# Kernel optimization log

Hardware: AMD Instinct MI355X
Metric: run time of the kernel (lower is better)

## Reference

```python
import jax, jax.numpy as jnp
import numpy as np

B, S, T, D = 4, 512, 512, 256


def setup_inputs() -> dict:
    key = jax.random.key(0)
    ks = jax.random.split(key, 10)
    scale = 1.0 / np.sqrt(D)
    return {
        "source": jax.random.normal(ks[0], (B, S, D), jnp.float32),
        "target": jax.random.normal(ks[1], (B, T, D), jnp.float32),
        "W_src": jax.random.uniform(ks[2], (D, D), jnp.float32, -scale, scale),
        "b_src": jax.random.uniform(ks[3], (D,), jnp.float32, -scale, scale),
        "W_tgt": jax.random.uniform(ks[4], (D, D), jnp.float32, -scale, scale),
        "b_tgt": jax.random.uniform(ks[5], (D,), jnp.float32, -scale, scale),
        "W_res": jax.random.uniform(ks[6], (D, 1), jnp.float32, -scale, scale),
        "b_res": jax.random.uniform(ks[7], (1,), jnp.float32, -scale, scale),
        "W_prob": jax.random.uniform(ks[8], (D, 2), jnp.float32, -scale, scale),
        "b_prob": jax.random.uniform(ks[9], (2,), jnp.float32, -scale, scale),
    }


def reference(source, target, W_src, b_src, W_tgt, b_tgt, W_res, b_res, W_prob, b_prob):
    # source: (B,S,D), target: (B,T,D)
    src_lin = jnp.einsum("bsd,de->bse", source, W_src) + b_src  # (B,S,D)
    tgt_lin = jnp.einsum("btd,de->bte", target, W_tgt) + b_tgt  # (B,T,D)
    # Bahdanau-style additive attention: (B,T,S,D) broadcast, tanh, D->1
    h = jnp.tanh(src_lin[:, None, :, :] + tgt_lin[:, :, None, :])  # (B,T,S,D)
    genP = jnp.einsum("btsd,d->bts", h, W_res[:, 0]) + b_res[0]     # (B,T,S)
    prob = jax.nn.softmax(jnp.einsum("btd,de->bte", target, W_prob) + b_prob, axis=-1)  # (B,T,2)
    return genP, prob
```

## Files before the change

### kernel.cpp

```cpp
#include <hip/hip_runtime.h>

#define B_ 4
#define S_ 512
#define T_ 512
#define D_ 256
#define NSRC (B_ * S_)
#define K2F 2.8853900817779268f

typedef __attribute__((ext_vector_type(8))) short short8;
typedef __attribute__((ext_vector_type(4))) float f32x4;
typedef __attribute__((ext_vector_type(2))) float f32x2;

__device__ __forceinline__ unsigned short f2bf(float f) {
    union { float f; unsigned u; } v; v.f = f;
    unsigned r = v.u + 0x7FFF + ((v.u >> 16) & 1);
    return (unsigned short)(r >> 16);
}

__global__ __launch_bounds__(256) void prep_kernel(
    const float* __restrict__ tgt,
    const float* __restrict__ Wsrc, const float* __restrict__ Wtgt,
    const float* __restrict__ Wp, const float* __restrict__ bp,
    unsigned short* __restrict__ wtb, float* __restrict__ out)
{
    __shared__ float tl[64 * 65];
    const int blk = blockIdx.x, tid = threadIdx.x;

    if (blk < 32) {
        int wb = blk;
        int e = wb >> 4, ti = wb & 15, tr = ti >> 2, tc = ti & 3;
        int r0 = tr * 64, c0 = tc * 64;
        const float* W = e ? Wtgt : Wsrc;
        #pragma unroll
        for (int it = 0; it < 4; it++) {
            int rr = (tid >> 4) + it * 16;
            int cc = (tid & 15) * 4;
            float4 v = *(const float4*)&W[(r0 + rr) * D_ + c0 + cc];
            tl[(cc + 0) * 65 + rr] = v.x;
            tl[(cc + 1) * 65 + rr] = v.y;
            tl[(cc + 2) * 65 + rr] = v.z;
            tl[(cc + 3) * 65 + rr] = v.w;
        }
        __syncthreads();
        #pragma unroll
        for (int it = 0; it < 2; it++) {
            int jj = (tid >> 3) + it * 32;
            int kk = (tid & 7) * 8;
            ushort4 lo, hi;
            lo.x = f2bf(tl[jj * 65 + kk + 0]); lo.y = f2bf(tl[jj * 65 + kk + 1]);
            lo.z = f2bf(tl[jj * 65 + kk + 2]); lo.w = f2bf(tl[jj * 65 + kk + 3]);
            hi.x = f2bf(tl[jj * 65 + kk + 4]); hi.y = f2bf(tl[jj * 65 + kk + 5]);
            hi.z = f2bf(tl[jj * 65 + kk + 6]); hi.w = f2bf(tl[jj * 65 + kk + 7]);
            int idx = (e * 256 + c0 + jj) * D_ + r0 + kk;
            *(ushort4*)&wtb[idx] = lo;
            *(ushort4*)&wtb[idx + 4] = hi;
        }
    } else {
        int row  = (blk - 32) * 4 + (tid >> 6);
        int lane = tid & 63;
        float p0 = 0.f, p1 = 0.f;
        #pragma unroll
        for (int i = 0; i < 4; i++) {
            int d = lane + i * 64;
            float v = tgt[row * D_ + d];
            float2 w = *(const float2*)&Wp[d * 2];
            p0 = fmaf(v, w.x, p0);
            p1 = fmaf(v, w.y, p1);
        }
        #pragma unroll
        for (int off = 32; off > 0; off >>= 1) {
            p0 += __shfl_down(p0, off, 64);
            p1 += __shfl_down(p1, off, 64);
        }
        if (lane == 0) {
            const float L2E = 1.4426950408889634f;
            float l0 = p0 + bp[0], l1 = p1 + bp[1];
            float e10 = __builtin_amdgcn_exp2f((l1 - l0) * L2E);
            float e01 = __builtin_amdgcn_exp2f((l0 - l1) * L2E);
            out[B_ * T_ * S_ + row * 2 + 0] = __builtin_amdgcn_rcpf(1.f + e10);
            out[B_ * T_ * S_ + row * 2 + 1] = __builtin_amdgcn_rcpf(1.f + e01);
        }
    }
}

#define LSTR 68
__global__ __launch_bounds__(768, 1) void mega_kernel(
    const float* __restrict__ src, const float* __restrict__ tgt,
    const unsigned short* __restrict__ wtb,
    const float* __restrict__ bsrc, const float* __restrict__ btgt,
    const float* __restrict__ Wres, const float* __restrict__ bres,
    float* __restrict__ out)
{
    __shared__ float ls[2][64 * LSTR];
    __shared__ float lt[2][64 * LSTR];
    __shared__ float c0s;

    const int tid = threadIdx.x;
    const int lane = tid & 63, w = tid >> 6;
    const int s0 = blockIdx.x * 64;
    const int t0 = blockIdx.y * 64;
    const int b  = blockIdx.z;

    if (w == 0) {
        float s = Wres[lane] + Wres[lane + 64] + Wres[lane + 128] + Wres[lane + 192];
        #pragma unroll
        for (int off = 32; off > 0; off >>= 1) s += __shfl_xor(s, off, 64);
        if (lane == 0) c0s = s + bres[0];
    }

    const bool producer = (w < 4);

    const int pw  = w & 3;
    const int mat = pw >> 1;
    const int rb  = 2 * (pw & 1);
    const int n = lane & 15, quad = lane >> 4;
    const float* bias = mat ? btgt : bsrc;
    const unsigned short* wtbase = wtb + mat * 256 * D_;

    short8 af[2][8];
    if (producer) {
        const float* xb = mat ? &tgt[(b * T_ + t0) * D_] : &src[(b * S_ + s0) * D_];
        #pragma unroll
        for (int rg = 0; rg < 2; rg++)
            #pragma unroll
            for (int ks = 0; ks < 8; ks++) {
                const float* p = &xb[((rb + rg) * 16 + n) * D_ + ks * 32 + quad * 8];
                float4 u0 = *(const float4*)p;
                float4 u1 = *(const float4*)(p + 4);
                short8 v;
                v[0] = (short)f2bf(u0.x); v[1] = (short)f2bf(u0.y);
                v[2] = (short)f2bf(u0.z); v[3] = (short)f2bf(u0.w);
                v[4] = (short)f2bf(u1.x); v[5] = (short)f2bf(u1.y);
                v[6] = (short)f2bf(u1.z); v[7] = (short)f2bf(u1.w);
                af[rg][ks] = v;
            }
    }

    auto phaseA = [&](int c, int bi) {
        float* lx = (mat ? lt[bi] : ls[bi]);
        #pragma unroll
        for (int cg = 0; cg < 4; cg++) {
            const int gcol = c * 4 + cg;
            const unsigned short* bptr = &wtbase[(gcol * 16 + n) * D_ + quad * 8];
            short8 bf[8];
            #pragma unroll
            for (int ks = 0; ks < 8; ks++) bf[ks] = *(const short8*)&bptr[ks * 32];
            const int dloc = cg * 16 + n;
            const float bv = bias[gcol * 16 + n];
            #pragma unroll
            for (int rg = 0; rg < 2; rg++) {
                f32x4 a4 = {0.f, 0.f, 0.f, 0.f};
                #pragma unroll
                for (int ks = 0; ks < 8; ks++)
                    a4 = __builtin_amdgcn_mfma_f32_16x16x32_bf16(af[rg][ks], bf[ks], a4, 0, 0, 0);
                float4 o;
                o.x = __builtin_amdgcn_exp2f((a4[0] + bv) * K2F);
                o.y = __builtin_amdgcn_exp2f((a4[1] + bv) * K2F);
                o.z = __builtin_amdgcn_exp2f((a4[2] + bv) * K2F);
                o.w = __builtin_amdgcn_exp2f((a4[3] + bv) * K2F);
                *(float4*)&lx[dloc * LSTR + (rb + rg) * 16 + quad * 4] = o;
            }
        }
    };

    const int cl = tid - 256;
    const int m = cl & 15;
    const int g = cl >> 4;
    f32x2 acc[2][2];
    #pragma unroll
    for (int i = 0; i < 2; i++) {
        acc[i][0] = (f32x2){0.f, 0.f};
        acc[i][1] = (f32x2){0.f, 0.f};
    }

    if (producer) phaseA(0, 0);
    __syncthreads();

    for (int c = 0; c < 4; c++) {
        const int bi = c & 1;
        if (producer) {
            if (c < 3) phaseA(c + 1, bi ^ 1);
        } else {
            const float* lsb = ls[bi];
            const float* ltb = lt[bi];
            const float* wp = &Wres[c * 64];
            const f32x2 one2 = {1.f, 1.f};
            #pragma unroll 2
            for (int kq = 0; kq < 8; kq++) {
                const int d0 = 8 * kq;
                f32x2 ap[8][2];
                float cc[8][2];
                f32x2 wv[8];
                #pragma unroll
                for (int k = 0; k < 8; k++) {
                    float4 a4 = *(const float4*)&lsb[(d0 + k) * LSTR + 4 * m];
                    float2 c2 = *(const float2*)&ltb[(d0 + k) * LSTR + 2 * g];
                    ap[k][0] = (f32x2){a4.x, a4.y};
                    ap[k][1] = (f32x2){a4.z, a4.w};
                    cc[k][0] = c2.x; cc[k][1] = c2.y;
                    const float wk = wp[d0 + k];
                    wv[k] = (f32x2){wk, wk};
                }
                #pragma unroll
                for (int i = 0; i < 2; i++) {
                    #pragma unroll
                    for (int jp = 0; jp < 2; jp++) {
                        f32x2 dd[8];
                        #pragma unroll
                        for (int k = 0; k < 8; k++) {
                            const f32x2 cs = {cc[k][i], cc[k][i]};
                            dd[k] = ap[k][jp] * cs + one2;
                        }
                        f32x2 p01 = dd[0] * dd[1];
                        f32x2 p23 = dd[2] * dd[3];
                        f32x2 p45 = dd[4] * dd[5];
                        f32x2 p67 = dd[6] * dd[7];
                        f32x2 q03 = p01 * p23;
                        f32x2 q47 = p45 * p67;
                        f32x2 den = q03 * q47;
                        f32x2 u01 = dd[1] * wv[0]; u01 = dd[0] * wv[1] + u01;
                        f32x2 u23 = dd[3] * wv[2]; u23 = dd[2] * wv[3] + u23;
                        f32x2 u45 = dd[5] * wv[4]; u45 = dd[4] * wv[5] + u45;
                        f32x2 u67 = dd[7] * wv[6]; u67 = dd[6] * wv[7] + u67;
                        f32x2 n03 = u01 * p23; n03 = u23 * p01 + n03;
                        f32x2 n47 = u45 * p67; n47 = u67 * p45 + n47;
                        f32x2 num = n03 * q47; num = n47 * q03 + num;
                        f32x2 r;
                        r.x = __builtin_amdgcn_rcpf(den.x);
                        r.y = __builtin_amdgcn_rcpf(den.y);
                        acc[i][jp] = num * r + acc[i][jp];
                    }
                }
            }
        }
        __syncthreads();
    }

    if (!producer) {
        const float C0 = c0s;
        #pragma unroll
        for (int i = 0; i < 2; i++) {
            float4 o;
            o.x = C0 - 2.f * acc[i][0].x;
            o.y = C0 - 2.f * acc[i][0].y;
            o.z = C0 - 2.f * acc[i][1].x;
            o.w = C0 - 2.f * acc[i][1].y;
            *(float4*)&out[(b * T_ + t0 + 2 * g + i) * S_ + s0 + 4 * m] = o;
        }
    }
}

extern "C" void kernel_launch(void* const* d_in, const int* in_sizes, int n_in,
                              void* d_out, int out_size, void* d_ws, size_t ws_size,
                              hipStream_t stream) {
    const float* source = (const float*)d_in[0];
    const float* target = (const float*)d_in[1];
    const float* W_src  = (const float*)d_in[2];
    const float* b_src  = (const float*)d_in[3];
    const float* W_tgt  = (const float*)d_in[4];
    const float* b_tgt  = (const float*)d_in[5];
    const float* W_res  = (const float*)d_in[6];
    const float* b_res  = (const float*)d_in[7];
    const float* W_prob = (const float*)d_in[8];
    const float* b_prob = (const float*)d_in[9];
    float* out = (float*)d_out;

    unsigned short* wtb = (unsigned short*)d_ws;

    prep_kernel<<<544, 256, 0, stream>>>(target, W_src, W_tgt,
                                         W_prob, b_prob, wtb, out);
    mega_kernel<<<dim3(8, 8, 4), 768, 0, stream>>>(source, target, wtb,
                                                   b_src, b_tgt,
                                                   W_res, b_res, out);
}
```

Before: 107.6 us.

## Split fused mega kernel into projection kernel and pairwise genP kernel

Replaces the producer/consumer mega kernel, which recomputed the exp of the source and target projections in every 64x64 tile, with a separate MFMA kernel. That kernel computes the exp'd projections once for all rows and writes them transposed to workspace. A new genP kernel uses 32x32 tiles with 256 threads, stages the workspace through double-buffered LDS with register prefetch, and runs the rational tanh-sum evaluation. This removes the redundant projection work and yields 1024 smaller blocks for better occupancy. In exchange it adds an extra launch and a global round trip for the intermediate.

```diff
diff --git a/kernel.cpp b/kernel.cpp
--- a/kernel.cpp
+++ b/kernel.cpp
@@ -5,6 +5,7 @@
 #define T_ 512
 #define D_ 256
 #define NSRC (B_ * S_)
+#define NROW 4096
 #define K2F 2.8853900817779268f
 
 typedef __attribute__((ext_vector_type(8))) short short8;
@@ -83,23 +84,76 @@
     }
 }
 
-#define LSTR 68
-__global__ __launch_bounds__(768, 1) void mega_kernel(
+__global__ __launch_bounds__(256) void ysyt_kernel(
     const float* __restrict__ src, const float* __restrict__ tgt,
     const unsigned short* __restrict__ wtb,
     const float* __restrict__ bsrc, const float* __restrict__ btgt,
+    float* __restrict__ yst)
+{
+    const int bx = blockIdx.x;
+    const int rowblk = bx >> 2, colq = bx & 3;
+    const int R0 = rowblk * 64;
+    const int tid = threadIdx.x, lane = tid & 63, w = tid >> 6;
+    const int n = lane & 15, quad = lane >> 4;
+    const int mat = (R0 >= NSRC) ? 1 : 0;
+    const float* bias = mat ? btgt : bsrc;
+    const unsigned short* wtbase = wtb + mat * 256 * D_;
+    const float* xb = mat ? &tgt[(R0 - NSRC) * D_] : &src[R0 * D_];
+
+    short8 af[8];
+    #pragma unroll
+    for (int ks = 0; ks < 8; ks++) {
+        const float* p = &xb[(w * 16 + n) * D_ + ks * 32 + quad * 8];
+        float4 u0 = *(const float4*)p;
+        float4 u1 = *(const float4*)(p + 4);
+        short8 v;
+        v[0] = (short)f2bf(u0.x); v[1] = (short)f2bf(u0.y);
+        v[2] = (short)f2bf(u0.z); v[3] = (short)f2bf(u0.w);
+        v[4] = (short)f2bf(u1.x); v[5] = (short)f2bf(u1.y);
+        v[6] = (short)f2bf(u1.z); v[7] = (short)f2bf(u1.w);
+        af[ks] = v;
+    }
+
+    #pragma unroll
+    for (int gc = 0; gc < 4; gc++) {
+        const int gcol = colq * 4 + gc;
+        const unsigned short* bptr = &wtbase[(gcol * 16 + n) * D_ + quad * 8];
+        short8 bf[8];
+        #pragma unroll
+        for (int ks = 0; ks < 8; ks++) bf[ks] = *(const short8*)&bptr[ks * 32];
+        f32x4 a4 = {0.f, 0.f, 0.f, 0.f};
+        #pragma unroll
+        for (int ks = 0; ks < 8; ks++)
+            a4 = __builtin_amdgcn_mfma_f32_16x16x32_bf16(af[ks], bf[ks], a4, 0, 0, 0);
+        const float bv = bias[gcol * 16 + n];
+        float4 o;
+        o.x = __builtin_amdgcn_exp2f((a4[0] + bv) * K2F);
+        o.y = __builtin_amdgcn_exp2f((a4[1] + bv) * K2F);
+        o.z = __builtin_amdgcn_exp2f((a4[2] + bv) * K2F);
+        o.w = __builtin_amdgcn_exp2f((a4[3] + bv) * K2F);
+        *(float4*)&yst[(gcol * 16 + n) * NROW + R0 + w * 16 + quad * 4] = o;
+    }
+}
+
+#define CLS 36
+__global__ __launch_bounds__(256) void genp_kernel(
+    const float* __restrict__ yst,
     const float* __restrict__ Wres, const float* __restrict__ bres,
     float* __restrict__ out)
 {
-    __shared__ float ls[2][64 * LSTR];
-    __shared__ float lt[2][64 * LSTR];
+    __shared__ float lys[2][64][CLS];
+    __shared__ float lyt[2][64][CLS];
     __shared__ float c0s;
 
     const int tid = threadIdx.x;
     const int lane = tid & 63, w = tid >> 6;
-    const int s0 = blockIdx.x * 64;
-    const int t0 = blockIdx.y * 64;
+    const int s0 = blockIdx.x * 32;
+    const int t0 = blockIdx.y * 32;
     const int b  = blockIdx.z;
+    const int m = tid & 15;
+    const int g = tid >> 4;
+    const int r = tid >> 3;
+    const int q = tid & 7;
 
     if (w == 0) {
         float s = Wres[lane] + Wres[lane + 64] + Wres[lane + 128] + Wres[lane + 192];
@@ -108,145 +162,100 @@
         if (lane == 0) c0s = s + bres[0];
     }
 
-    const bool producer = (w < 4);
-
-    const int pw  = w & 3;
-    const int mat = pw >> 1;
-    const int rb  = 2 * (pw & 1);
-    const int n = lane & 15, quad = lane >> 4;
-    const float* bias = mat ? btgt : bsrc;
-    const unsigned short* wtbase = wtb + mat * 256 * D_;
-
-    short8 af[2][8];
-    if (producer) {
-        const float* xb = mat ? &tgt[(b * T_ + t0) * D_] : &src[(b * S_ + s0) * D_];
-        #pragma unroll
-        for (int rg = 0; rg < 2; rg++)
+    const int ysbase = b * S_ + s0;
+    const int ytbase = NSRC + b * T_ + t0;
+
+    {
+        float4 a0 = *(const float4*)&yst[(r)      * NROW + ysbase + 4 * q];
+        float4 a1 = *(const float4*)&yst[(r + 32) * NROW + ysbase + 4 * q];
+        float4 b0 = *(const float4*)&yst[(r)      * NROW + ytbase + 4 * q];
+        float4 b1 = *(const float4*)&yst[(r + 32) * NROW + ytbase + 4 * q];
+        *(float4*)&lys[0][r][4 * q]      = a0;
+        *(float4*)&lys[0][r + 32][4 * q] = a1;
+        *(float4*)&lyt[0][r][4 * q]      = b0;
+        *(float4*)&lyt[0][r + 32][4 * q] = b1;
+    }
+    __syncthreads();
+
+    f32x2 acc[2];
+    acc[0] = (f32x2){0.f, 0.f};
+    acc[1] = (f32x2){0.f, 0.f};
+    const f32x2 one2 = {1.f, 1.f};
+
+    for (int c = 0; c < 4; c++) {
+        const int bi = c & 1;
+        float4 pa0, pa1, pb0, pb1;
+        if (c < 3) {
+            const int dn = (c + 1) * 64;
+            pa0 = *(const float4*)&yst[(dn + r)      * NROW + ysbase + 4 * q];
+            pa1 = *(const float4*)&yst[(dn + r + 32) * NROW + ysbase + 4 * q];
+            pb0 = *(const float4*)&yst[(dn + r)      * NROW + ytbase + 4 * q];
+            pb1 = *(const float4*)&yst[(dn + r + 32) * NROW + ytbase + 4 * q];
+        }
+
+        const float* wp = &Wres[c * 64];
+        #pragma unroll 2
+        for (int kq = 0; kq < 8; kq++) {
+            const int d0 = 8 * kq;
+            f32x2 ap[8];
+            float2 ct[8];
+            f32x2 wv[8];
             #pragma unroll
-            for (int ks = 0; ks < 8; ks++) {
-                const float* p = &xb[((rb + rg) * 16 + n) * D_ + ks * 32 + quad * 8];
-                float4 u0 = *(const float4*)p;
-                float4 u1 = *(const float4*)(p + 4);
-                short8 v;
-                v[0] = (short)f2bf(u0.x); v[1] = (short)f2bf(u0.y);
-                v[2] = (short)f2bf(u0.z); v[3] = (short)f2bf(u0.w);
-                v[4] = (short)f2bf(u1.x); v[5] = (short)f2bf(u1.y);
-                v[6] = (short)f2bf(u1.z); v[7] = (short)f2bf(u1.w);
-                af[rg][ks] = v;
+            for (int k = 0; k < 8; k++) {
+                float2 a2 = *(const float2*)&lys[bi][d0 + k][2 * m];
+                ct[k] = *(const float2*)&lyt[bi][d0 + k][2 * g];
+                ap[k] = (f32x2){a2.x, a2.y};
+                const float wk = wp[d0 + k];
+                wv[k] = (f32x2){wk, wk};
             }
-    }
-
-    auto phaseA = [&](int c, int bi) {
-        float* lx = (mat ? lt[bi] : ls[bi]);
-        #pragma unroll
-        for (int cg = 0; cg < 4; cg++) {
-            const int gcol = c * 4 + cg;
-            const unsigned short* bptr = &wtbase[(gcol * 16 + n) * D_ + quad * 8];
-            short8 bf[8];
             #pragma unroll
-            for (int ks = 0; ks < 8; ks++) bf[ks] = *(const short8*)&bptr[ks * 32];
-            const int dloc = cg * 16 + n;
-            const float bv = bias[gcol * 16 + n];
-            #pragma unroll
-            for (int rg = 0; rg < 2; rg++) {
-                f32x4 a4 = {0.f, 0.f, 0.f, 0.f};
+            for (int i = 0; i < 2; i++) {
+                const float c0 = i ? ct[0].y : ct[0].x;
+                f32x2 dd[8];
                 #pragma unroll
-                for (int ks = 0; ks < 8; ks++)
-                    a4 = __builtin_amdgcn_mfma_f32_16x16x32_bf16(af[rg][ks], bf[ks], a4, 0, 0, 0);
-                float4 o;
-                o.x = __builtin_amdgcn_exp2f((a4[0] + bv) * K2F);
-                o.y = __builtin_amdgcn_exp2f((a4[1] + bv) * K2F);
-                o.z = __builtin_amdgcn_exp2f((a4[2] + bv) * K2F);
-                o.w = __builtin_amdgcn_exp2f((a4[3] + bv) * K2F);
-                *(float4*)&lx[dloc * LSTR + (rb + rg) * 16 + quad * 4] = o;
+                for (int k = 0; k < 8; k++) {
+                    const float cv = i ? ct[k].y : ct[k].x;
+                    const f32x2 cs = {cv, cv};
+                    dd[k] = ap[k] * cs + one2;
+                }
+                f32x2 p01 = dd[0] * dd[1];
+                f32x2 p23 = dd[2] * dd[3];
+                f32x2 p45 = dd[4] * dd[5];
+                f32x2 p67 = dd[6] * dd[7];
+                f32x2 q03 = p01 * p23;
+                f32x2 q47 = p45 * p67;
+                f32x2 den = q03 * q47;
+                f32x2 u01 = dd[1] * wv[0]; u01 = dd[0] * wv[1] + u01;
+                f32x2 u23 = dd[3] * wv[2]; u23 = dd[2] * wv[3] + u23;
+                f32x2 u45 = dd[5] * wv[4]; u45 = dd[4] * wv[5] + u45;
+                f32x2 u67 = dd[7] * wv[6]; u67 = dd[6] * wv[7] + u67;
+                f32x2 n03 = u01 * p23; n03 = u23 * p01 + n03;
+                f32x2 n47 = u45 * p67; n47 = u67 * p45 + n47;
+                f32x2 num = n03 * q47; num = n47 * q03 + num;
+                f32x2 rr;
+                rr.x = __builtin_amdgcn_rcpf(den.x);
+                rr.y = __builtin_amdgcn_rcpf(den.y);
+                acc[i] = num * rr + acc[i];
+                (void)c0;
             }
         }
-    };
-
-    const int cl = tid - 256;
-    const int m = cl & 15;
-    const int g = cl >> 4;
-    f32x2 acc[2][2];
+
+        if (c < 3) {
+            *(float4*)&lys[bi ^ 1][r][4 * q]      = pa0;
+            *(float4*)&lys[bi ^ 1][r + 32][4 * q] = pa1;
+            *(float4*)&lyt[bi ^ 1][r][4 * q]      = pb0;
+            *(float4*)&lyt[bi ^ 1][r + 32][4 * q] = pb1;
+        }
+        __syncthreads();
+    }
+
+    const float C0 = c0s;
     #pragma unroll
     for (int i = 0; i < 2; i++) {
-        acc[i][0] = (f32x2){0.f, 0.f};
-        acc[i][1] = (f32x2){0.f, 0.f};
-    }
-
-    if (producer) phaseA(0, 0);
-    __syncthreads();
-
-    for (int c = 0; c < 4; c++) {
-        const int bi = c & 1;
-        if (producer) {
-            if (c < 3) phaseA(c + 1, bi ^ 1);
-        } else {
-            const float* lsb = ls[bi];
-            const float* ltb = lt[bi];
-            const float* wp = &Wres[c * 64];
-            const f32x2 one2 = {1.f, 1.f};
-            #pragma unroll 2
-            for (int kq = 0; kq < 8; kq++) {
-                const int d0 = 8 * kq;
-                f32x2 ap[8][2];
-                float cc[8][2];
-                f32x2 wv[8];
-                #pragma unroll
-                for (int k = 0; k < 8; k++) {
-                    float4 a4 = *(const float4*)&lsb[(d0 + k) * LSTR + 4 * m];
-                    float2 c2 = *(const float2*)&ltb[(d0 + k) * LSTR + 2 * g];
-                    ap[k][0] = (f32x2){a4.x, a4.y};
-                    ap[k][1] = (f32x2){a4.z, a4.w};
-                    cc[k][0] = c2.x; cc[k][1] = c2.y;
-                    const float wk = wp[d0 + k];
-                    wv[k] = (f32x2){wk, wk};
-                }
-                #pragma unroll
-                for (int i = 0; i < 2; i++) {
-                    #pragma unroll
-                    for (int jp = 0; jp < 2; jp++) {
-                        f32x2 dd[8];
-                        #pragma unroll
-                        for (int k = 0; k < 8; k++) {
-                            const f32x2 cs = {cc[k][i], cc[k][i]};
-                            dd[k] = ap[k][jp] * cs + one2;
-                        }
-                        f32x2 p01 = dd[0] * dd[1];
-                        f32x2 p23 = dd[2] * dd[3];
-                        f32x2 p45 = dd[4] * dd[5];
-                        f32x2 p67 = dd[6] * dd[7];
-                        f32x2 q03 = p01 * p23;
-                        f32x2 q47 = p45 * p67;
-                        f32x2 den = q03 * q47;
-                        f32x2 u01 = dd[1] * wv[0]; u01 = dd[0] * wv[1] + u01;
-                        f32x2 u23 = dd[3] * wv[2]; u23 = dd[2] * wv[3] + u23;
-                        f32x2 u45 = dd[5] * wv[4]; u45 = dd[4] * wv[5] + u45;
-                        f32x2 u67 = dd[7] * wv[6]; u67 = dd[6] * wv[7] + u67;
-                        f32x2 n03 = u01 * p23; n03 = u23 * p01 + n03;
-                        f32x2 n47 = u45 * p67; n47 = u67 * p45 + n47;
-                        f32x2 num = n03 * q47; num = n47 * q03 + num;
-                        f32x2 r;
-                        r.x = __builtin_amdgcn_rcpf(den.x);
-                        r.y = __builtin_amdgcn_rcpf(den.y);
-                        acc[i][jp] = num * r + acc[i][jp];
-                    }
-                }
-            }
-        }
-        __syncthreads();
-    }
-
-    if (!producer) {
-        const float C0 = c0s;
-        #pragma unroll
-        for (int i = 0; i < 2; i++) {
-            float4 o;
-            o.x = C0 - 2.f * acc[i][0].x;
-            o.y = C0 - 2.f * acc[i][0].y;
-            o.z = C0 - 2.f * acc[i][1].x;
-            o.w = C0 - 2.f * acc[i][1].y;
-            *(float4*)&out[(b * T_ + t0 + 2 * g + i) * S_ + s0 + 4 * m] = o;
-        }
+        float2 o;
+        o.x = C0 - 2.f * acc[i].x;
+        o.y = C0 - 2.f * acc[i].y;
+        *(float2*)&out[(b * T_ + t0 + 2 * g + i) * S_ + s0 + 2 * m] = o;
     }
 }
 
@@ -266,10 +275,11 @@
     float* out = (float*)d_out;
 
     unsigned short* wtb = (unsigned short*)d_ws;
+    float* yst = (float*)((char*)d_ws + 256 * 1024);
 
     prep_kernel<<<544, 256, 0, stream>>>(target, W_src, W_tgt,
                                          W_prob, b_prob, wtb, out);
-    mega_kernel<<<dim3(8, 8, 4), 768, 0, stream>>>(source, target, wtb,
-                                                   b_src, b_tgt,
-                                                   W_res, b_res, out);
-}
+    ysyt_kernel<<<256, 256, 0, stream>>>(source, target, wtb,
+                                         b_src, b_tgt, yst);
+    genp_kernel<<<dim3(16, 16, 4), 256, 0, stream>>>(yst, W_res, b_res, out);
+}
```

New measurement: 107.1 us. Within noise of the previous version (-0.4%).
